# Kernel optimization log

Measured on AMD Instinct MI355X. Metric: run time of the kernel, lower is better.

The kernel has to match this reference:

```python
import jax, jax.numpy as jnp
import numpy as np

B, S, H, D = 1, 4096, 16, 64   # batch, seq_len, heads, dim_head (hidden = H*D = 1024)
Q_CHUNK = 512                  # query chunk size; divides S


def setup_inputs() -> dict:
    key = jax.random.key(0)
    kq, kk, kv = jax.random.split(key, 3)
    shape = (B, S, H * D)
    return {
        "query": jax.random.normal(kq, shape, jnp.float32),
        "key": jax.random.normal(kk, shape, jnp.float32),
        "value": jax.random.normal(kv, shape, jnp.float32),
    }


def _heads_to_batch(x):
    # (b, s, h*d) -> (b*h, s, d), matching reshape_heads_to_batch_dim
    b, s, _ = x.shape
    return x.reshape(b, s, H, D).transpose(0, 2, 1, 3).reshape(b * H, s, D)


def _batch_to_heads(x, b):
    # (b*h, s, d) -> (b, s, h*d), matching reshape_batch_dim_to_heads
    bh, s, d = x.shape
    return x.reshape(b, H, s, d).transpose(0, 2, 1, 3).reshape(b, s, H * d)


def reference(query, key, value):
    """Memory-efficient attention path of AttentionOp.apply_attention_dot.

    Math: out = softmax(q k^T / sqrt(dim_head)) v per (batch*head).
    (The mem-efficient path scales by 1/sqrt(k_features); self.scale is unused there.)
    Computed in query chunks to avoid materializing the full [BH, S, S] scores,
    honoring the chunked structure of the original.
    """
    b = query.shape[0]
    q = _heads_to_batch(query) * (1.0 / jnp.sqrt(jnp.float32(D)))  # (BH, S, D)
    k = _heads_to_batch(key)
    v = _heads_to_batch(value)

    n_chunks = q.shape[1] // Q_CHUNK
    # (n_chunks, BH, Q_CHUNK, D)
    qc = q.reshape(-1, n_chunks, Q_CHUNK, D).transpose(1, 0, 2, 3)

    def attend_chunk(qi):
        scores = jnp.einsum("bqd,bkd->bqk", qi, k)        # (BH, C, S)
        probs = jax.nn.softmax(scores, axis=-1)           # stable online-softmax equiv.
        return jnp.einsum("bqk,bkd->bqd", probs, v)       # (BH, C, D)

    oc = jax.lax.map(attend_chunk, qc)                    # (n_chunks, BH, C, D)
    out = oc.transpose(1, 0, 2, 3).reshape(-1, n_chunks * Q_CHUNK, D)
    return _batch_to_heads(out, b)
```

## Files before the change

### kernel.cpp

```cpp
#include <hip/hip_runtime.h>
#include <stdint.h>

typedef __bf16 bf16;
typedef __bf16 bf16x8 __attribute__((ext_vector_type(8)));
typedef float  f32x16 __attribute__((ext_vector_type(16)));

#define S_LEN 4096
#define NHEAD 16
#define HID   1024
#define NTILE 64
#define TILEB 8192
#define QSCALE (0.125f * 1.44269504088896340736f)
#define EXP2F(x) __builtin_amdgcn_exp2f(x)

__device__ __forceinline__ uint32_t pack_bf16(float a, float b) {
    union { bf16 h[2]; uint32_t u; } x;
    x.h[0] = (bf16)a; x.h[1] = (bf16)b;
    return x.u;
}

__global__ __launch_bounds__(256)
void prepack_kernel(const float* __restrict__ Kg, const float* __restrict__ Vg,
                    char* __restrict__ Kb, char* __restrict__ Vb)
{
    const int tile = blockIdx.x, h = blockIdx.y;
    const int t = threadIdx.x;
    __shared__ float Vs[64][65];

    const int key = t >> 2, dq = (t & 3) * 16;
    const float* kp = Kg + (size_t)(tile * 64 + key) * HID + h * 64 + dq;
    const float* vp = Vg + (size_t)(tile * 64 + key) * HID + h * 64 + dq;
    float kv[16], vv[16];
    #pragma unroll
    for (int i = 0; i < 4; ++i) {
        *(float4*)(kv + 4 * i) = *(const float4*)(kp + 4 * i);
        *(float4*)(vv + 4 * i) = *(const float4*)(vp + 4 * i);
    }
    {
        char* kout = Kb + (size_t)(h * NTILE + tile) * TILEB;
        const int i = (t & 3) * 2 + (key >> 5);
        bf16x8 b0, b1;
        #pragma unroll
        for (int e = 0; e < 8; ++e) { b0[e] = (bf16)kv[e]; b1[e] = (bf16)kv[8 + e]; }
        *(bf16x8*)(kout + i * 1024 + (key & 31) * 16)        = b0;
        *(bf16x8*)(kout + i * 1024 + (32 + (key & 31)) * 16) = b1;
    }
    #pragma unroll
    for (int e = 0; e < 16; ++e) Vs[key][dq + e] = vv[e];
    __syncthreads();
    {
        const int d = t >> 2, kq = (t & 3) * 16;
        float tv[16];
        #pragma unroll
        for (int e = 0; e < 16; ++e) tv[e] = Vs[kq + e][d];
        char* vout = Vb + (size_t)(h * NTILE + tile) * TILEB;
        const int j = (t & 3) * 2 + (d >> 5);
        bf16x8 b0, b1;
        #pragma unroll
        for (int e = 0; e < 8; ++e) { b0[e] = (bf16)tv[e]; b1[e] = (bf16)tv[8 + e]; }
        *(bf16x8*)(vout + j * 1024 + (d & 31) * 16)        = b0;
        *(bf16x8*)(vout + j * 1024 + (32 + (d & 31)) * 16) = b1;
    }
}

__global__ __launch_bounds__(256, 4)
void fattn_kernel(const float* __restrict__ Qg,
                  const char* __restrict__ Kb,
                  const char* __restrict__ Vb,
                  float* __restrict__ Og)
{
    const int sb = (blockIdx.x & 7) * 128 + (blockIdx.x >> 3);
    const int h  = sb >> 6;
    const int qc = sb & 63;
    const int t  = threadIdx.x;
    const int w  = t >> 6;
    const int qg = w >> 1;
    const int ws = w & 1;
    const int l  = t & 63;
    const int lq = l & 31;
    const int hi = l >> 5;

    __shared__ __attribute__((aligned(16))) float part[2 * 64 * 33];
    char* const obuf = (char*)part;

    bf16x8 qf[4];
    {
        const float* qp = Qg + (size_t)(qc * 64 + qg * 32 + lq) * HID + h * 64 + hi * 8;
        #pragma unroll
        for (int kc = 0; kc < 4; ++kc) {
            float tmp[8];
            *(float4*)(tmp)     = *(const float4*)(qp + kc * 16);
            *(float4*)(tmp + 4) = *(const float4*)(qp + kc * 16 + 4);
            #pragma unroll
            for (int e = 0; e < 8; ++e) qf[kc][e] = (bf16)(tmp[e] * QSCALE);
        }
    }

    f32x16 ot0, ot1;
    #pragma unroll
    for (int i = 0; i < 16; ++i) { ot0[i] = 0.f; ot1[i] = 0.f; }
    float lrun = 0.f;

    const char* Khead = Kb + (size_t)h * (NTILE * TILEB) + (size_t)ws * 32 * TILEB;
    const char* Vhead = Vb + (size_t)h * (NTILE * TILEB) + (size_t)ws * 32 * TILEB;

    for (int it = 0; it < 32; ++it) {
        const char* kt = Khead + (size_t)it * TILEB;
        const char* vt = Vhead + (size_t)it * TILEB;

        #pragma unroll
        for (int khalf = 0; khalf < 2; ++khalf) {
            bf16x8 kfh[4];
            #pragma unroll
            for (int kc = 0; kc < 4; ++kc)
                kfh[kc] = *(const bf16x8*)(kt + (kc * 2 + khalf) * 1024 + l * 16);

            f32x16 sc;
            #pragma unroll
            for (int i = 0; i < 16; ++i) sc[i] = 0.f;
            __builtin_amdgcn_s_setprio(1);
            #pragma unroll
            for (int kc = 0; kc < 4; ++kc)
                sc = __builtin_amdgcn_mfma_f32_32x32x16_bf16(kfh[kc], qf[kc], sc, 0, 0, 0);
            __builtin_amdgcn_s_setprio(0);

            bf16x8 vfh[4];
            #pragma unroll
            for (int j = 0; j < 4; ++j)
                vfh[j] = *(const bf16x8*)(vt + (khalf * 4 + j) * 1024 + l * 16);

            {
                float pa = 0.f, pb = 0.f, pc = 0.f, pd = 0.f;
                #pragma unroll
                for (int i = 0; i < 16; i += 4) {
                    float p0 = EXP2F(sc[i]),     p1 = EXP2F(sc[i + 1]);
                    float p2 = EXP2F(sc[i + 2]), p3 = EXP2F(sc[i + 3]);
                    sc[i] = p0; sc[i + 1] = p1; sc[i + 2] = p2; sc[i + 3] = p3;
                    pa += p0; pb += p1; pc += p2; pd += p3;
                }
                lrun += (pa + pb) + (pc + pd);
            }

            auto pvchunk = [&](int eb, const bf16x8& v0, const bf16x8& v1) {
                uint32_t p0 = pack_bf16(sc[eb + 0], sc[eb + 1]);
                uint32_t p1 = pack_bf16(sc[eb + 2], sc[eb + 3]);
                uint32_t p2 = pack_bf16(sc[eb + 4], sc[eb + 5]);
                uint32_t p3 = pack_bf16(sc[eb + 6], sc[eb + 7]);
                asm volatile("v_permlane32_swap_b32 %0, %1" : "+v"(p0), "+v"(p2));
                asm volatile("v_permlane32_swap_b32 %0, %1" : "+v"(p1), "+v"(p3));
                union { uint32_t w4[4]; bf16x8 v; } pb;
                pb.w4[0] = p0; pb.w4[1] = p1; pb.w4[2] = p2; pb.w4[3] = p3;
                __builtin_amdgcn_s_setprio(1);
                ot0 = __builtin_amdgcn_mfma_f32_32x32x16_bf16(v0, pb.v, ot0, 0, 0, 0);
                ot1 = __builtin_amdgcn_mfma_f32_32x32x16_bf16(v1, pb.v, ot1, 0, 0, 0);
                __builtin_amdgcn_s_setprio(0);
            };
            pvchunk(0, vfh[0], vfh[1]);
            pvchunk(8, vfh[2], vfh[3]);
        }
    }

    lrun += __shfl_xor(lrun, 32);

    if (ws == 1) {
        float* pp = part + (qg * 64 + l) * 33;
        #pragma unroll
        for (int r = 0; r < 16; ++r) { pp[r] = ot0[r]; pp[16 + r] = ot1[r]; }
        pp[32] = lrun;
    }
    __syncthreads();
    if (ws == 0) {
        const float* pp = part + (qg * 64 + l) * 33;
        #pragma unroll
        for (int r = 0; r < 16; ++r) { ot0[r] += pp[r]; ot1[r] += pp[16 + r]; }
        lrun += pp[32];
    }
    __syncthreads();
    if (ws == 0) {
        const float inv = 1.f / lrun;
        char* ob = obuf + qg * 8192;
        const int x = (lq & 7) << 4;
        #pragma unroll
        for (int r = 0; r < 16; ++r) {
            const int d0 = (r & 3) + 8 * (r >> 2) + 4 * hi;
            *(float*)(ob + ((lq * 256 + d0 * 4) ^ x))        = ot0[r] * inv;
            *(float*)(ob + ((lq * 256 + (32 + d0) * 4) ^ x)) = ot1[r] * inv;
        }
    }
    __syncthreads();
    {
        const int row = t >> 2, quarter = t & 3;
        const int qloc = row & 31;
        const int x = (qloc & 7) << 4;
        const char* ob = obuf + (row >> 5) * 8192;
        float* op = Og + (size_t)(qc * 64 + row) * HID + h * 64 + quarter * 16;
        #pragma unroll
        for (int i = 0; i < 4; ++i) {
            float4 v = *(const float4*)(ob + ((qloc * 256 + quarter * 64 + i * 16) ^ x));
            *(float4*)(op + i * 4) = v;
        }
    }
}

extern "C" void kernel_launch(void* const* d_in, const int* in_sizes, int n_in,
                              void* d_out, int out_size, void* d_ws, size_t ws_size,
                              hipStream_t stream) {
    const float* Q = (const float*)d_in[0];
    const float* K = (const float*)d_in[1];
    const float* V = (const float*)d_in[2];
    float* O = (float*)d_out;
    char* Kb = (char*)d_ws;
    char* Vb = (char*)d_ws + (size_t)NHEAD * NTILE * TILEB;
    dim3 pgrid(NTILE, NHEAD);
    prepack_kernel<<<pgrid, 256, 0, stream>>>(K, V, Kb, Vb);
    fattn_kernel<<<1024, 256, 0, stream>>>(Q, Kb, Vb, O);
}
```

Measured before the change: 107.2 us.

## Share K/V tiles across 8 waves via async LDS staging pipeline

Each block now holds 512 threads covering 256 queries, replacing the previous 256-thread, 64-query blocks. All eight waves iterate the full key range and read K/V tiles from LDS, which are staged through global_load_lds into a 4-slot ring buffer, two tiles ahead. Previously each wave read bf16 K/V fragments straight from global memory, and the key range was split across wave pairs that then needed an LDS reduction. The change cuts global/L2 traffic by reusing each tile across 8 query groups, at the cost of two barriers per tile, fewer blocks (256), and lower occupancy.

```diff
diff --git a/kernel.cpp b/kernel.cpp
--- a/kernel.cpp
+++ b/kernel.cpp
@@ -12,6 +12,13 @@
 #define TILEB 8192
 #define QSCALE (0.125f * 1.44269504088896340736f)
 #define EXP2F(x) __builtin_amdgcn_exp2f(x)
+
+#define AS1 __attribute__((address_space(1)))
+#define AS3 __attribute__((address_space(3)))
+
+__device__ __forceinline__ void gload16(const void* g, void* l) {
+    __builtin_amdgcn_global_load_lds((const AS1 uint32_t*)g, (AS3 uint32_t*)l, 16, 0, 0);
+}
 
 __device__ __forceinline__ uint32_t pack_bf16(float a, float b) {
     union { bf16 h[2]; uint32_t u; } x;
@@ -63,29 +70,26 @@
     }
 }
 
-__global__ __launch_bounds__(256, 4)
+__global__ __launch_bounds__(512, 2)
 void fattn_kernel(const float* __restrict__ Qg,
                   const char* __restrict__ Kb,
                   const char* __restrict__ Vb,
                   float* __restrict__ Og)
 {
-    const int sb = (blockIdx.x & 7) * 128 + (blockIdx.x >> 3);
-    const int h  = sb >> 6;
-    const int qc = sb & 63;
+    const int sb = (blockIdx.x & 7) * 32 + (blockIdx.x >> 3);
+    const int h  = sb >> 4;
+    const int qc = sb & 15;
     const int t  = threadIdx.x;
     const int w  = t >> 6;
-    const int qg = w >> 1;
-    const int ws = w & 1;
     const int l  = t & 63;
     const int lq = l & 31;
     const int hi = l >> 5;
 
-    __shared__ __attribute__((aligned(16))) float part[2 * 64 * 33];
-    char* const obuf = (char*)part;
+    __shared__ __attribute__((aligned(128))) char lds[4 * 16384];
 
     bf16x8 qf[4];
     {
-        const float* qp = Qg + (size_t)(qc * 64 + qg * 32 + lq) * HID + h * 64 + hi * 8;
+        const float* qp = Qg + (size_t)(qc * 256 + w * 32 + lq) * HID + h * 64 + hi * 8;
         #pragma unroll
         for (int kc = 0; kc < 4; ++kc) {
             float tmp[8];
@@ -101,12 +105,34 @@
     for (int i = 0; i < 16; ++i) { ot0[i] = 0.f; ot1[i] = 0.f; }
     float lrun = 0.f;
 
-    const char* Khead = Kb + (size_t)h * (NTILE * TILEB) + (size_t)ws * 32 * TILEB;
-    const char* Vhead = Vb + (size_t)h * (NTILE * TILEB) + (size_t)ws * 32 * TILEB;
-
-    for (int it = 0; it < 32; ++it) {
-        const char* kt = Khead + (size_t)it * TILEB;
-        const char* vt = Vhead + (size_t)it * TILEB;
+    const int sw = w & 3;
+    const char* const srcb = ((w < 4) ? Kb : Vb)
+                           + (size_t)h * (NTILE * TILEB) + sw * 2048 + l * 16;
+    const int dstoff = (w < 4 ? 0 : 8192) + sw * 2048;
+    auto stage = [&](int tile) {
+        const char* src = srcb + (size_t)tile * TILEB;
+        char* dst = lds + (tile & 3) * 16384 + dstoff;
+        gload16(src, dst);
+        gload16(src + 1024, dst + 1024);
+    };
+
+    stage(0);
+    stage(1);
+
+    for (int it = 0; it < NTILE; ++it) {
+        if (it < NTILE - 2) {
+            stage(it + 2);
+            asm volatile("s_waitcnt vmcnt(4)" ::: "memory");
+        } else if (it == NTILE - 2) {
+            asm volatile("s_waitcnt vmcnt(2)" ::: "memory");
+        } else {
+            asm volatile("s_waitcnt vmcnt(0)" ::: "memory");
+        }
+        __builtin_amdgcn_s_barrier();
+        asm volatile("" ::: "memory");
+
+        const char* kt = lds + (it & 3) * 16384;
+        const char* vt = kt + 8192;
 
         #pragma unroll
         for (int khalf = 0; khalf < 2; ++khalf) {
@@ -158,27 +184,18 @@
             pvchunk(0, vfh[0], vfh[1]);
             pvchunk(8, vfh[2], vfh[3]);
         }
+
+        __builtin_amdgcn_s_barrier();
+        asm volatile("" ::: "memory");
     }
 
     lrun += __shfl_xor(lrun, 32);
 
-    if (ws == 1) {
-        float* pp = part + (qg * 64 + l) * 33;
-        #pragma unroll
-        for (int r = 0; r < 16; ++r) { pp[r] = ot0[r]; pp[16 + r] = ot1[r]; }
-        pp[32] = lrun;
-    }
     __syncthreads();
-    if (ws == 0) {
-        const float* pp = part + (qg * 64 + l) * 33;
-        #pragma unroll
-        for (int r = 0; r < 16; ++r) { ot0[r] += pp[r]; ot1[r] += pp[16 + r]; }
-        lrun += pp[32];
-    }
-    __syncthreads();
-    if (ws == 0) {
+
+    {
+        char* const ob = lds + w * 8192;
         const float inv = 1.f / lrun;
-        char* ob = obuf + qg * 8192;
         const int x = (lq & 7) << 4;
         #pragma unroll
         for (int r = 0; r < 16; ++r) {
@@ -186,17 +203,12 @@
             *(float*)(ob + ((lq * 256 + d0 * 4) ^ x))        = ot0[r] * inv;
             *(float*)(ob + ((lq * 256 + (32 + d0) * 4) ^ x)) = ot1[r] * inv;
         }
-    }
-    __syncthreads();
-    {
-        const int row = t >> 2, quarter = t & 3;
-        const int qloc = row & 31;
-        const int x = (qloc & 7) << 4;
-        const char* ob = obuf + (row >> 5) * 8192;
-        float* op = Og + (size_t)(qc * 64 + row) * HID + h * 64 + quarter * 16;
-        #pragma unroll
-        for (int i = 0; i < 4; ++i) {
-            float4 v = *(const float4*)(ob + ((qloc * 256 + quarter * 64 + i * 16) ^ x));
+        const int row = l >> 1, half = l & 1;
+        const int xr = (row & 7) << 4;
+        float* op = Og + (size_t)(qc * 256 + w * 32 + row) * HID + h * 64 + half * 32;
+        #pragma unroll
+        for (int i = 0; i < 8; ++i) {
+            float4 v = *(const float4*)(ob + ((row * 256 + half * 128 + i * 16) ^ xr));
             *(float4*)(op + i * 4) = v;
         }
     }
@@ -213,5 +225,5 @@
     char* Vb = (char*)d_ws + (size_t)NHEAD * NTILE * TILEB;
     dim3 pgrid(NTILE, NHEAD);
     prepack_kernel<<<pgrid, 256, 0, stream>>>(K, V, Kb, Vb);
-    fattn_kernel<<<1024, 256, 0, stream>>>(Q, Kb, Vb, O);
-}
+    fattn_kernel<<<256, 512, 0, stream>>>(Q, Kb, Vb, O);
+}
```

After: 99.50 us. -7.2%, faster.
